# Kernel tuning notes

Measured on AMD Instinct MI355X. Metric: run time of the kernel, lower is better.

## Reference

```python
import jax, jax.numpy as jnp
import numpy as np

IN_CH = 512
HID = 512
SCALE = 1.0 / np.sqrt(16.0)  # hard-coded 16**0.5 in source, not sqrt(hidden)


def setup_inputs() -> dict:
    key = jax.random.key(0)
    ks = jax.random.split(key, 9)
    B, T = 8, 2048
    lim = 1.0 / np.sqrt(IN_CH)
    return {
        "q": jax.random.normal(ks[0], (B, T, IN_CH), dtype=jnp.float32),
        "k": jax.random.normal(ks[1], (B, T, IN_CH), dtype=jnp.float32),
        "v": jax.random.normal(ks[2], (B, T, IN_CH), dtype=jnp.float32),
        "Wq": jax.random.uniform(ks[3], (IN_CH, HID), jnp.float32, -lim, lim),
        "bq": jax.random.uniform(ks[4], (HID,), jnp.float32, -lim, lim),
        "Wk": jax.random.uniform(ks[5], (IN_CH, HID), jnp.float32, -lim, lim),
        "bk": jax.random.uniform(ks[6], (HID,), jnp.float32, -lim, lim),
        "Wv": jax.random.uniform(ks[7], (IN_CH, HID), jnp.float32, -lim, lim),
        "bv": jax.random.uniform(ks[8], (HID,), jnp.float32, -lim, lim),
    }


def reference(q, k, v, Wq, bq, Wk, bk, Wv, bv):
    # Linear projections: [B,T,F] @ [F,H] + [H]
    query = jnp.einsum("btf,fh->bth", q, Wq) + bq
    key_p = jnp.einsum("btf,fh->bth", k, Wk) + bk
    value = jnp.einsum("btf,fh->bth", v, Wv) + bv
    # energy: [B,T,T], scaled by fixed 1/sqrt(16)
    energy = jnp.einsum("bth,bsh->bts", query, key_p) * SCALE
    attn = jax.nn.softmax(energy, axis=-1)
    # weighted sum: [B,T,H]
    return jnp.einsum("bts,bsh->bth", attn, value)
```

## Files before the change

kernel.cpp:

```cpp
#include <hip/hip_runtime.h>
#include <stdint.h>

typedef __bf16 bf16;
typedef bf16 bf16x8 __attribute__((ext_vector_type(8)));
typedef float f32x4 __attribute__((ext_vector_type(4)));

#define MFMA(a, b, c) __builtin_amdgcn_mfma_f32_16x16x32_bf16(a, b, c, 0, 0, 0)

#define SCALE_L2E 0.3606737602222409f
#define M0 16.0f

#define WAITVM0 asm volatile("s_waitcnt vmcnt(0)" ::: "memory")
#define WAITLGKM0 asm volatile("s_waitcnt lgkmcnt(0)" ::: "memory")
#define SBAR __builtin_amdgcn_s_barrier()
#define SCHEDB __builtin_amdgcn_sched_barrier(0)
#define PRIO(x) __builtin_amdgcn_s_setprio(x)

__device__ __forceinline__ void gload_lds16(const void* g, void* l) {
  __builtin_amdgcn_global_load_lds(
      (const __attribute__((address_space(1))) uint32_t*)g,
      (__attribute__((address_space(3))) uint32_t*)l, 16, 0, 0);
}

__global__ void k_wtrans(const float* __restrict__ Wq, const float* __restrict__ Wk,
                         const float* __restrict__ Wv, bf16* __restrict__ Wt) {
  __shared__ float tile[32][33];
  int x = threadIdx.x, y = threadIdx.y;
  int k0 = blockIdx.x * 32, n0 = blockIdx.y * 32, z = blockIdx.z;
  const float* W = (z == 0) ? Wq : (z == 1) ? Wk : Wv;
  for (int j = 0; j < 4; j++)
    tile[y + 8 * j][x] = W[(size_t)(k0 + y + 8 * j) * 512 + n0 + x];
  __syncthreads();
  bf16* o = Wt + (size_t)z * 262144;
  for (int j = 0; j < 4; j++)
    o[(size_t)(n0 + y + 8 * j) * 512 + k0 + x] = (bf16)tile[x][y + 8 * j];
}

__global__ __launch_bounds__(256, 2) void k_proj(
    const float* __restrict__ q, const float* __restrict__ k, const float* __restrict__ v,
    const bf16* __restrict__ Wt, const float* __restrict__ bq, const float* __restrict__ bk,
    const float* __restrict__ bv, bf16* __restrict__ Qp, bf16* __restrict__ Kp,
    bf16* __restrict__ Vtp) {
  int z = blockIdx.z;
  const float* A = (z == 0) ? q : (z == 1) ? k : v;
  const float* bias = (z == 0) ? bq : (z == 1) ? bk : bv;
  const bf16* Bw = Wt + (size_t)z * 262144;

  int m0 = blockIdx.x * 128, n0 = blockIdx.y * 128;
  __shared__ __align__(16) char smem[65536];
  bf16* As = (bf16*)smem;
  bf16* Bs = (bf16*)(smem + 32768);
  bf16* Ts = (bf16*)smem;

  int tid = threadIdx.x;
  int wave = tid >> 6, lane = tid & 63, qr = lane & 15, quad = lane >> 4;
  int wm = (wave >> 1) * 64, wn = (wave & 1) * 64;

  f32x4 acc[4][4];
  for (int mi = 0; mi < 4; mi++)
    for (int ni = 0; ni < 4; ni++) acc[mi][ni] = (f32x4){0.f, 0.f, 0.f, 0.f};

  float4 rx[4], ry[4];

  auto issue = [&](int kk, int buf) {
#pragma unroll
    for (int i = 0; i < 4; i++) {
      int ch = i * 256 + tid, row = ch >> 3, c = ch & 7;
      const float4* src = (const float4*)(A + (size_t)(m0 + row) * 512 + kk + c * 8);
      rx[i] = src[0];
      ry[i] = src[1];
    }
#pragma unroll
    for (int i = 0; i < 4; i++) {
      int ch = i * 256 + tid, row = ch >> 3, c = ch & 7, cs = c ^ (row & 7);
      gload_lds16(Bw + (size_t)(n0 + row) * 512 + kk + cs * 8, &Bs[buf * 8192 + ch * 8]);
    }
  };

  auto writeA = [&](int buf) {
#pragma unroll
    for (int i = 0; i < 4; i++) {
      int ch = i * 256 + tid, row = ch >> 3, c = ch & 7, cs = c ^ (row & 7);
      bf16x8 t;
      t[0] = (bf16)rx[i].x; t[1] = (bf16)rx[i].y; t[2] = (bf16)rx[i].z; t[3] = (bf16)rx[i].w;
      t[4] = (bf16)ry[i].x; t[5] = (bf16)ry[i].y; t[6] = (bf16)ry[i].z; t[7] = (bf16)ry[i].w;
      *(bf16x8*)&As[buf * 8192 + row * 64 + cs * 8] = t;
    }
  };

  auto compute = [&](int buf) {
    bf16* Ab = &As[buf * 8192];
    bf16* Bb = &Bs[buf * 8192];
#pragma unroll
    for (int h = 0; h < 2; h++) {
      bf16x8 af[4], bfv[4];
#pragma unroll
      for (int mi = 0; mi < 4; mi++) {
        int rr = wm + mi * 16 + qr;
        int cc = (h * 4 + quad) ^ (rr & 7);
        af[mi] = *(bf16x8*)&Ab[rr * 64 + cc * 8];
      }
#pragma unroll
      for (int ni = 0; ni < 4; ni++) {
        int rr = wn + ni * 16 + qr;
        int cc = (h * 4 + quad) ^ (rr & 7);
        bfv[ni] = *(bf16x8*)&Bb[rr * 64 + cc * 8];
      }
#pragma unroll
      for (int mi = 0; mi < 4; mi++)
#pragma unroll
        for (int ni = 0; ni < 4; ni++) acc[mi][ni] = MFMA(af[mi], bfv[ni], acc[mi][ni]);
    }
  };

  issue(0, 0);
  writeA(0);
  __syncthreads();

  int cur = 0;
  for (int t = 0; t < 8; t++) {
    if (t < 7) issue((t + 1) * 64, cur ^ 1);
    compute(cur);
    if (t < 7) writeA(cur ^ 1);
    __syncthreads();
    cur ^= 1;
  }

  if (z == 2) {
    for (int ni = 0; ni < 4; ni++) {
      int hcol = wn + ni * 16 + qr;
      float bz = bias[n0 + hcol];
      for (int mi = 0; mi < 4; mi++) {
        int tl = wm + mi * 16 + quad * 4;
        bf16 tmp[4];
        for (int r = 0; r < 4; r++) tmp[r] = (bf16)(acc[mi][ni][r] + bz);
        *(uint64_t*)&Ts[hcol * 136 + tl] = *(uint64_t*)tmp;
      }
    }
    __syncthreads();
    int bb = m0 >> 11, t0l = m0 & 2047;
    for (int i = 0; i < 8; i++) {
      int ch = i * 256 + tid;
      int row = ch >> 4, c = ch & 15;
      *(bf16x8*)(Vtp + (size_t)(bb * 512 + n0 + row) * 2048 + t0l + c * 8) =
          *(bf16x8*)&Ts[row * 136 + c * 8];
    }
  } else {
    bf16* C = (z == 0) ? Qp : Kp;
    float sc = (z == 0) ? SCALE_L2E : 1.0f;
    for (int ni = 0; ni < 4; ni++) {
      int col = n0 + wn + ni * 16 + qr;
      float bz = bias[col];
      for (int mi = 0; mi < 4; mi++) {
        int rbase = m0 + wm + mi * 16 + quad * 4;
        for (int r = 0; r < 4; r++)
          C[(size_t)(rbase + r) * 512 + col] = (bf16)((acc[mi][ni][r] + bz) * sc);
      }
    }
  }
}

__global__ __launch_bounds__(512, 1) void k_qk(const bf16* __restrict__ Qp,
                                               const bf16* __restrict__ Kp,
                                               bf16* __restrict__ P,
                                               float* __restrict__ Lpart) {
  __shared__ __align__(16) bf16 S[65536];
  int b = blockIdx.z;
  const bf16* A = Qp + (size_t)b * 2048 * 512;
  const bf16* B = Kp + (size_t)b * 2048 * 512;
  bf16* Pb = P + (size_t)b * 2048 * 2048;
  int m0 = blockIdx.x * 256, n0 = blockIdx.y * 256;
  int tid = threadIdx.x;
  int wave = tid >> 6, lane = tid & 63, qr = lane & 15, quad = lane >> 4;
  int wm = wave >> 2, wn = wave & 3;

  f32x4 acc[8][4];
  for (int mi = 0; mi < 8; mi++)
    for (int ni = 0; ni < 4; ni++) acc[mi][ni] = (f32x4){0.f, 0.f, 0.f, 0.f};

  auto stage = [&](int t, int s) {
    int kk = t * 64;
    bf16* As_ = S + s * 16384;
    bf16* Bs_ = S + 32768 + s * 16384;
#pragma unroll
    for (int j = 0; j < 4; j++) {
      int ch = j * 512 + tid, row = ch >> 3, c = ch & 7, cs = c ^ (row & 7);
      gload_lds16(A + (size_t)(m0 + row) * 512 + kk + cs * 8, As_ + ch * 8);
    }
#pragma unroll
    for (int j = 0; j < 4; j++) {
      int ch = j * 512 + tid, row = ch >> 3, c = ch & 7, cs = c ^ (row & 7);
      gload_lds16(B + (size_t)(n0 + row) * 512 + kk + cs * 8, Bs_ + ch * 8);
    }
  };

  stage(0, 0);
  WAITVM0;
  SBAR;

  for (int t = 0; t < 8; t++) {
    int cur = t & 1;
    bf16* As_ = S + cur * 16384;
    bf16* Bs_ = S + 32768 + cur * 16384;

    if (t < 7) stage(t + 1, cur ^ 1);
    bf16x8 aF[4][2], bF[4][2];
#pragma unroll
    for (int mi = 0; mi < 4; mi++)
#pragma unroll
      for (int kk = 0; kk < 2; kk++) {
        int row = wm * 128 + mi * 16 + qr;
        aF[mi][kk] = *(bf16x8*)&As_[row * 64 + ((kk * 4 + quad) ^ (row & 7)) * 8];
      }
#pragma unroll
    for (int ni = 0; ni < 4; ni++)
#pragma unroll
      for (int kk = 0; kk < 2; kk++) {
        int row = wn * 64 + ni * 16 + qr;
        bF[ni][kk] = *(bf16x8*)&Bs_[row * 64 + ((kk * 4 + quad) ^ (row & 7)) * 8];
      }
    SBAR;
    WAITLGKM0;
    SCHEDB;
    PRIO(1);
#pragma unroll
    for (int kk = 0; kk < 2; kk++)
#pragma unroll
      for (int mi = 0; mi < 4; mi++)
#pragma unroll
        for (int ni = 0; ni < 4; ni++)
          acc[mi][ni] = MFMA(aF[mi][kk], bF[ni][kk], acc[mi][ni]);
    PRIO(0);
    SBAR;

#pragma unroll
    for (int mi = 0; mi < 4; mi++)
#pragma unroll
      for (int kk = 0; kk < 2; kk++) {
        int row = wm * 128 + 64 + mi * 16 + qr;
        aF[mi][kk] = *(bf16x8*)&As_[row * 64 + ((kk * 4 + quad) ^ (row & 7)) * 8];
      }
    SBAR;
    WAITLGKM0;
    SCHEDB;
    PRIO(1);
#pragma unroll
    for (int kk = 0; kk < 2; kk++)
#pragma unroll
      for (int mi = 0; mi < 4; mi++)
#pragma unroll
        for (int ni = 0; ni < 4; ni++)
          acc[4 + mi][ni] = MFMA(aF[mi][kk], bF[ni][kk], acc[4 + mi][ni]);
    PRIO(0);
    WAITVM0;
    SBAR;
  }

  int slice = blockIdx.y * 4 + wn;
  float* Lp = Lpart + (size_t)slice * 16384 + b * 2048;
#pragma unroll
  for (int mi = 0; mi < 8; mi++) {
    int rowb = m0 + wm * 128 + mi * 16 + quad * 4;
#pragma unroll
    for (int r = 0; r < 4; r++) {
      float s = 0.f;
      bf16* prow = Pb + (size_t)(rowb + r) * 2048 + n0 + wn * 64 + qr;
#pragma unroll
      for (int ni = 0; ni < 4; ni++) {
        float e = exp2f(acc[mi][ni][r] - M0);
        prow[ni * 16] = (bf16)e;
        s += e;
      }
      s += __shfl_xor(s, 1);
      s += __shfl_xor(s, 2);
      s += __shfl_xor(s, 4);
      s += __shfl_xor(s, 8);
      if (qr == 0) Lp[rowb + r] = s;
    }
  }
}

__global__ __launch_bounds__(512, 1) void k_pv(const bf16* __restrict__ P,
                                               const bf16* __restrict__ Vtp,
                                               const float* __restrict__ Lpart,
                                               float* __restrict__ out) {
  __shared__ __align__(16) bf16 S[49152];
  int b = blockIdx.z;
  const bf16* A = P + (size_t)b * 2048 * 2048;
  const bf16* B = Vtp + (size_t)b * 512 * 2048;
  int m0 = blockIdx.x * 256, n0 = blockIdx.y * 128;
  int tid = threadIdx.x;
  int wave = tid >> 6, lane = tid & 63, qr = lane & 15, quad = lane >> 4;
  int wmi = wave >> 1, wni = wave & 1;

  float linv_own = 0.f;
  if (tid < 256) {
    float s = 0.f;
    for (int j = 0; j < 32; j++) s += Lpart[(size_t)j * 16384 + b * 2048 + m0 + tid];
    linv_own = 1.0f / s;
  }

  f32x4 acc[4][4];
  for (int mi = 0; mi < 4; mi++)
    for (int ni = 0; ni < 4; ni++) acc[mi][ni] = (f32x4){0.f, 0.f, 0.f, 0.f};

  auto stage = [&](int t, int s) {
    int kk = t * 64;
    bf16* As_ = S + s * 16384;
    bf16* Bs_ = S + 32768 + s * 8192;
#pragma unroll
    for (int j = 0; j < 4; j++) {
      int ch = j * 512 + tid, row = ch >> 3, c = ch & 7, cs = c ^ (row & 7);
      gload_lds16(A + (size_t)(m0 + row) * 2048 + kk + cs * 8, As_ + ch * 8);
    }
#pragma unroll
    for (int j = 0; j < 2; j++) {
      int ch = j * 512 + tid, row = ch >> 3, c = ch & 7, cs = c ^ (row & 7);
      gload_lds16(B + (size_t)(n0 + row) * 2048 + kk + cs * 8, Bs_ + ch * 8);
    }
  };

  stage(0, 0);
  WAITVM0;
  SBAR;

  for (int t = 0; t < 32; t++) {
    int cur = t & 1;
    bf16* As_ = S + cur * 16384;
    bf16* Bs_ = S + 32768 + cur * 8192;

    if (t < 31) stage(t + 1, cur ^ 1);
    bf16x8 aF[2][2], bF[4][2];
#pragma unroll
    for (int mi = 0; mi < 2; mi++)
#pragma unroll
      for (int kk = 0; kk < 2; kk++) {
        int row = wmi * 64 + mi * 16 + qr;
        aF[mi][kk] = *(bf16x8*)&As_[row * 64 + ((kk * 4 + quad) ^ (row & 7)) * 8];
      }
#pragma unroll
    for (int ni = 0; ni < 4; ni++)
#pragma unroll
      for (int kk = 0; kk < 2; kk++) {
        int row = wni * 64 + ni * 16 + qr;
        bF[ni][kk] = *(bf16x8*)&Bs_[row * 64 + ((kk * 4 + quad) ^ (row & 7)) * 8];
      }
    SBAR;
    WAITLGKM0;
    SCHEDB;
    PRIO(1);
#pragma unroll
    for (int kk = 0; kk < 2; kk++)
#pragma unroll
      for (int mi = 0; mi < 2; mi++)
#pragma unroll
        for (int ni = 0; ni < 4; ni++)
          acc[mi][ni] = MFMA(aF[mi][kk], bF[ni][kk], acc[mi][ni]);
    PRIO(0);
    SBAR;

#pragma unroll
    for (int mi = 0; mi < 2; mi++)
#pragma unroll
      for (int kk = 0; kk < 2; kk++) {
        int row = wmi * 64 + 32 + mi * 16 + qr;
        aF[mi][kk] = *(bf16x8*)&As_[row * 64 + ((kk * 4 + quad) ^ (row & 7)) * 8];
      }
    SBAR;
    WAITLGKM0;
    SCHEDB;
    PRIO(1);
#pragma unroll
    for (int kk = 0; kk < 2; kk++)
#pragma unroll
      for (int mi = 0; mi < 2; mi++)
#pragma unroll
        for (int ni = 0; ni < 4; ni++)
          acc[2 + mi][ni] = MFMA(aF[mi][kk], bF[ni][kk], acc[2 + mi][ni]);
    PRIO(0);
    WAITVM0;
    SBAR;
  }

  float* Linv_s = (float*)S;
  if (tid < 256) Linv_s[tid] = linv_own;
  SBAR;

#pragma unroll
  for (int mi = 0; mi < 4; mi++) {
    int rowl = wmi * 64 + mi * 16 + quad * 4;
    float linv[4];
    for (int r = 0; r < 4; r++) linv[r] = Linv_s[rowl + r];
#pragma unroll
    for (int ni = 0; ni < 4; ni++) {
      int col = n0 + wni * 64 + ni * 16 + qr;
      float* og = out + (size_t)(b * 2048 + m0 + rowl) * 512 + col;
      for (int r = 0; r < 4; r++) og[(size_t)r * 512] = acc[mi][ni][r] * linv[r];
    }
  }
}

extern "C" void kernel_launch(void* const* d_in, const int* in_sizes, int n_in,
                              void* d_out, int out_size, void* d_ws, size_t ws_size,
                              hipStream_t stream) {
  (void)in_sizes; (void)n_in; (void)out_size; (void)ws_size;
  const float* q  = (const float*)d_in[0];
  const float* k  = (const float*)d_in[1];
  const float* v  = (const float*)d_in[2];
  const float* Wq = (const float*)d_in[3];
  const float* bq = (const float*)d_in[4];
  const float* Wk = (const float*)d_in[5];
  const float* bk = (const float*)d_in[6];
  const float* Wv = (const float*)d_in[7];
  const float* bv = (const float*)d_in[8];
  float* out = (float*)d_out;

  char* ws = (char*)d_ws;
  bf16* Wt     = (bf16*)(ws);
  bf16* Qp     = (bf16*)(ws + 1572864);
  bf16* Kp     = (bf16*)(ws + 18350080);
  bf16* Vtp    = (bf16*)(ws + 35127296);
  bf16* P      = (bf16*)(ws + 51904512);
  float* Lpart = (float*)(ws + 119013376);

  k_wtrans<<<dim3(16, 16, 3), dim3(32, 8, 1), 0, stream>>>(Wq, Wk, Wv, Wt);
  k_proj<<<dim3(128, 4, 3), 256, 0, stream>>>(q, k, v, Wt, bq, bk, bv, Qp, Kp, Vtp);
  k_qk<<<dim3(8, 8, 8), 512, 0, stream>>>(Qp, Kp, P, Lpart);
  k_pv<<<dim3(8, 4, 8), 512, 0, stream>>>(P, Vtp, Lpart, out);
}
```

Before: 267.7 us.

## Deepen async global-to-LDS prefetch with counted vmcnt waits across all GEMM kernels

Replaces full vmcnt(0) waits with counted partial waits so the next stage's global-to-LDS loads stay in flight while compute proceeds. In the QK and PV kernels the stage for t+2 is issued into the buffer just consumed, giving two stages in flight instead of one. The A-tile loads are reordered so the first half can be waited on early, and the PV kernel merges its two half-compute phases into one. In the projection kernel, sched barriers pin the load issue order and explicit waits replace syncthreads. The risk is a race if the vmcnt counts do not match the actual number of outstanding loads, plus higher register pressure from the larger fragment arrays.

```diff
diff --git a/kernel.cpp b/kernel.cpp
--- a/kernel.cpp
+++ b/kernel.cpp
@@ -10,7 +10,7 @@
 #define SCALE_L2E 0.3606737602222409f
 #define M0 16.0f
 
-#define WAITVM0 asm volatile("s_waitcnt vmcnt(0)" ::: "memory")
+#define WAITVM(N) asm volatile("s_waitcnt vmcnt(" #N ")" ::: "memory")
 #define WAITLGKM0 asm volatile("s_waitcnt lgkmcnt(0)" ::: "memory")
 #define SBAR __builtin_amdgcn_s_barrier()
 #define SCHEDB __builtin_amdgcn_sched_barrier(0)
@@ -70,11 +70,13 @@
       rx[i] = src[0];
       ry[i] = src[1];
     }
+    SCHEDB;
 #pragma unroll
     for (int i = 0; i < 4; i++) {
       int ch = i * 256 + tid, row = ch >> 3, c = ch & 7, cs = c ^ (row & 7);
       gload_lds16(Bw + (size_t)(n0 + row) * 512 + kk + cs * 8, &Bs[buf * 8192 + ch * 8]);
     }
+    SCHEDB;
   };
 
   auto writeA = [&](int buf) {
@@ -115,15 +117,19 @@
 
   issue(0, 0);
   writeA(0);
-  __syncthreads();
-
-  int cur = 0;
+  WAITLGKM0;
+  SBAR;
+
   for (int t = 0; t < 8; t++) {
+    int cur = t & 1;
     if (t < 7) issue((t + 1) * 64, cur ^ 1);
+    if (t < 7) { WAITVM(12); } else { WAITVM(0); }
+    SBAR;
+    SCHEDB;
     compute(cur);
     if (t < 7) writeA(cur ^ 1);
-    __syncthreads();
-    cur ^= 1;
+    WAITLGKM0;
+    SBAR;
   }
 
   if (z == 2) {
@@ -178,32 +184,36 @@
   for (int mi = 0; mi < 8; mi++)
     for (int ni = 0; ni < 4; ni++) acc[mi][ni] = (f32x4){0.f, 0.f, 0.f, 0.f};
 
+  auto stageAj = [&](int t, int s, int j) {
+    int kk = t * 64;
+    bf16* As_ = S + s * 16384;
+    int ch = j * 512 + tid, row = ch >> 3, c = ch & 7, cs = c ^ (row & 7);
+    gload_lds16(A + (size_t)(m0 + row) * 512 + kk + cs * 8, As_ + ch * 8);
+  };
   auto stage = [&](int t, int s) {
     int kk = t * 64;
-    bf16* As_ = S + s * 16384;
     bf16* Bs_ = S + 32768 + s * 16384;
-#pragma unroll
-    for (int j = 0; j < 4; j++) {
-      int ch = j * 512 + tid, row = ch >> 3, c = ch & 7, cs = c ^ (row & 7);
-      gload_lds16(A + (size_t)(m0 + row) * 512 + kk + cs * 8, As_ + ch * 8);
-    }
 #pragma unroll
     for (int j = 0; j < 4; j++) {
       int ch = j * 512 + tid, row = ch >> 3, c = ch & 7, cs = c ^ (row & 7);
       gload_lds16(B + (size_t)(n0 + row) * 512 + kk + cs * 8, Bs_ + ch * 8);
     }
+    stageAj(t, s, 0);
+    stageAj(t, s, 2);
+    stageAj(t, s, 1);
+    stageAj(t, s, 3);
   };
 
   stage(0, 0);
-  WAITVM0;
-  SBAR;
+  stage(1, 1);
 
   for (int t = 0; t < 8; t++) {
     int cur = t & 1;
     bf16* As_ = S + cur * 16384;
     bf16* Bs_ = S + 32768 + cur * 16384;
 
-    if (t < 7) stage(t + 1, cur ^ 1);
+    if (t < 7) { WAITVM(10); } else { WAITVM(2); }
+    SBAR;
     bf16x8 aF[4][2], bF[4][2];
 #pragma unroll
     for (int mi = 0; mi < 4; mi++)
@@ -219,7 +229,6 @@
         int row = wn * 64 + ni * 16 + qr;
         bF[ni][kk] = *(bf16x8*)&Bs_[row * 64 + ((kk * 4 + quad) ^ (row & 7)) * 8];
       }
-    SBAR;
     WAITLGKM0;
     SCHEDB;
     PRIO(1);
@@ -231,8 +240,9 @@
         for (int ni = 0; ni < 4; ni++)
           acc[mi][ni] = MFMA(aF[mi][kk], bF[ni][kk], acc[mi][ni]);
     PRIO(0);
-    SBAR;
-
+
+    if (t < 7) { WAITVM(8); } else { WAITVM(0); }
+    SBAR;
 #pragma unroll
     for (int mi = 0; mi < 4; mi++)
 #pragma unroll
@@ -240,8 +250,9 @@
         int row = wm * 128 + 64 + mi * 16 + qr;
         aF[mi][kk] = *(bf16x8*)&As_[row * 64 + ((kk * 4 + quad) ^ (row & 7)) * 8];
       }
-    SBAR;
     WAITLGKM0;
+    SBAR;
+    if (t < 6) stage(t + 2, cur);
     SCHEDB;
     PRIO(1);
 #pragma unroll
@@ -252,8 +263,6 @@
         for (int ni = 0; ni < 4; ni++)
           acc[4 + mi][ni] = MFMA(aF[mi][kk], bF[ni][kk], acc[4 + mi][ni]);
     PRIO(0);
-    WAITVM0;
-    SBAR;
   }
 
   int slice = blockIdx.y * 4 + wn;
@@ -321,18 +330,18 @@
   };
 
   stage(0, 0);
-  WAITVM0;
-  SBAR;
+  stage(1, 1);
 
   for (int t = 0; t < 32; t++) {
     int cur = t & 1;
     bf16* As_ = S + cur * 16384;
     bf16* Bs_ = S + 32768 + cur * 8192;
 
-    if (t < 31) stage(t + 1, cur ^ 1);
-    bf16x8 aF[2][2], bF[4][2];
-#pragma unroll
-    for (int mi = 0; mi < 2; mi++)
+    if (t < 31) { WAITVM(6); } else { WAITVM(0); }
+    SBAR;
+    bf16x8 aF[4][2], bF[4][2];
+#pragma unroll
+    for (int mi = 0; mi < 4; mi++)
 #pragma unroll
       for (int kk = 0; kk < 2; kk++) {
         int row = wmi * 64 + mi * 16 + qr;
@@ -345,43 +354,23 @@
         int row = wni * 64 + ni * 16 + qr;
         bF[ni][kk] = *(bf16x8*)&Bs_[row * 64 + ((kk * 4 + quad) ^ (row & 7)) * 8];
       }
-    SBAR;
     WAITLGKM0;
+    SBAR;
+    if (t < 30) stage(t + 2, cur);
     SCHEDB;
     PRIO(1);
 #pragma unroll
     for (int kk = 0; kk < 2; kk++)
 #pragma unroll
-      for (int mi = 0; mi < 2; mi++)
+      for (int mi = 0; mi < 4; mi++)
 #pragma unroll
         for (int ni = 0; ni < 4; ni++)
           acc[mi][ni] = MFMA(aF[mi][kk], bF[ni][kk], acc[mi][ni]);
     PRIO(0);
-    SBAR;
-
-#pragma unroll
-    for (int mi = 0; mi < 2; mi++)
-#pragma unroll
-      for (int kk = 0; kk < 2; kk++) {
-        int row = wmi * 64 + 32 + mi * 16 + qr;
-        aF[mi][kk] = *(bf16x8*)&As_[row * 64 + ((kk * 4 + quad) ^ (row & 7)) * 8];
-      }
-    SBAR;
-    WAITLGKM0;
-    SCHEDB;
-    PRIO(1);
-#pragma unroll
-    for (int kk = 0; kk < 2; kk++)
-#pragma unroll
-      for (int mi = 0; mi < 2; mi++)
-#pragma unroll
-        for (int ni = 0; ni < 4; ni++)
-          acc[2 + mi][ni] = MFMA(aF[mi][kk], bF[ni][kk], acc[2 + mi][ni]);
-    PRIO(0);
-    WAITVM0;
-    SBAR;
-  }
-
+  }
+
+  WAITLGKM0;
+  SBAR;
   float* Linv_s = (float*)S;
   if (tid < 256) Linv_s[tid] = linv_own;
   SBAR;
```

After: 262.3 us. -2.0%, faster.
